# Optimization experiments

Measured on AMD Instinct MI355X. Metric: run time of the kernel, lower is better.

The kernel has to match this reference:

```python
import jax, jax.numpy as jnp
import numpy as np

B, N, C, H = 2, 2048, 128, 4
C4 = C // 4


def setup_inputs() -> dict:
    key = jax.random.key(0)
    ks = jax.random.split(key, 20)
    s = 0.02
    f = lambda k, sh: (jax.random.normal(k, sh, jnp.float32) * s)
    return {
        'x': jax.random.normal(ks[0], (B, N, C), jnp.float32),
        'A': jax.random.randint(ks[1], (N, N), 0, 2).astype(jnp.int32),
        'q_w1': f(ks[2], (C, C)), 'kv_w1': f(ks[3], (2 * C, C)),
        'proj_w1': f(ks[4], (C, C)), 'proj_b1': jnp.zeros((C,), jnp.float32),
        'q_w2': f(ks[5], (C, C)), 'kv_w2': f(ks[6], (2 * C, C)),
        'proj_w2': f(ks[7], (C, C)), 'proj_b2': jnp.zeros((C,), jnp.float32),
        'cq_w': f(ks[8], (C4, C)), 'cq_b': jnp.zeros((C4,), jnp.float32),
        'ck_w': f(ks[9], (C4, C)), 'ck_b': jnp.zeros((C4,), jnp.float32),
        'cv_w': f(ks[10], (C, C)), 'cv_b': jnp.zeros((C,), jnp.float32),
        'gc_w': f(ks[11], (C, C)), 'gc_b': jnp.zeros((C,), jnp.float32),
    }


def _attn_block(x, A, qw, kvw, pw, pb):
    # Attention._inner_attention + residual; qkv_bias=False, scale=head_dim**-0.5
    b, n, c = x.shape
    hd = c // H
    q = (x @ qw.T).reshape(b, n, H, hd).transpose(0, 2, 1, 3)          # [B,H,N,hd]
    kv = (x @ kvw.T).reshape(b, n, 2, H, hd).transpose(2, 0, 3, 1, 4)  # [2,B,H,N,hd]
    k, v = kv[0], kv[1]
    attn = jnp.einsum('bhnd,bhmd->bhnm', q, k) * (hd ** -0.5)
    attn = jnp.where(A[None, None] > 0, attn, jnp.float32(-9e15))
    attn = jax.nn.softmax(attn, axis=-1)
    out = jnp.einsum('bhnm,bhmd->bhnd', attn, v).transpose(0, 2, 1, 3).reshape(b, n, c)
    return out @ pw.T + pb + x


def _graph_conv(x, cq_w, cq_b, ck_w, ck_b, cv_w, cv_b, gc_w, gc_b):
    # GraphConvolution.forward: conv1d(k=1) QKV, softmax, topk scatter mask, masked softmax, bmm
    b, s, c = x.shape
    xp = x.transpose(0, 2, 1)                                          # [B,C,N]
    query = jnp.einsum('oi,bin->bon', cq_w, xp) + cq_b[:, None]        # [B,C/4,N]
    keyt = (jnp.einsum('oi,bin->bon', ck_w, xp) + ck_b[:, None]).transpose(0, 2, 1)  # [B,N,C/4]
    adj = jax.nn.softmax(jnp.einsum('bnc,bcm->bnm', keyt, query), axis=-1)           # [B,N,N]
    kk = int(s / 3 * 2)                                                # top-2/3 per row
    _, idx = jax.lax.top_k(adj, kk)                                    # [B,N,kk]
    mask = jnp.zeros(adj.shape, bool).at[
        jnp.arange(b)[:, None, None], jnp.arange(s)[None, :, None], idx].set(True)
    adj = jax.nn.softmax(jnp.where(mask, adj, -jnp.inf), axis=-1)
    value = (jnp.einsum('oi,bin->bon', cv_w, xp) + cv_b[:, None]).transpose(0, 2, 1)  # [B,N,C]
    support = value @ gc_w
    return jnp.einsum('bnm,bmc->bnc', adj, support) + gc_b


def reference(x, A, q_w1, kv_w1, proj_w1, proj_b1, q_w2, kv_w2, proj_w2, proj_b2,
              cq_w, cq_b, ck_w, ck_b, cv_w, cv_b, gc_w, gc_b):
    x = _attn_block(x, A, q_w1, kv_w1, proj_w1, proj_b1)
    x = _attn_block(x, A, q_w2, kv_w2, proj_w2, proj_b2)
    return _graph_conv(x, cq_w, cq_b, ck_w, ck_b, cv_w, cv_b, gc_w, gc_b)
```

## Files before the change

### kernel.cpp

```cpp
#include <hip/hip_runtime.h>
#include <hip/hip_bf16.h>
#include <math.h>

#define BB 2
#define NN 2048
#define CC 128
#define HH 4
#define HD 32
#define KK_TOP 1365

typedef __attribute__((ext_vector_type(8))) short v8s;
typedef __attribute__((ext_vector_type(4))) float f32x4;

#define MFMA16(a, b, c) __builtin_amdgcn_mfma_f32_16x16x32_bf16(a, b, c, 0, 0, 0)

__device__ inline float wave_max_f(float v) {
    #pragma unroll
    for (int m = 1; m < 64; m <<= 1) v = fmaxf(v, __shfl_xor(v, m));
    return v;
}
__device__ inline float wave_min_f(float v) {
    #pragma unroll
    for (int m = 1; m < 64; m <<= 1) v = fminf(v, __shfl_xor(v, m));
    return v;
}
__device__ inline float wave_sum_f(float v) {
    #pragma unroll
    for (int m = 1; m < 64; m <<= 1) v += __shfl_xor(v, m);
    return v;
}
__device__ inline unsigned short bf16bits(float x) {
    __hip_bfloat16 h = __float2bfloat16(x);
    return *reinterpret_cast<unsigned short*>(&h);
}

__global__ __launch_bounds__(256) void prep_k(
    const int* __restrict__ A, unsigned* __restrict__ Ab2,
    const float* __restrict__ cv_w, const float* __restrict__ cv_b,
    const float* __restrict__ gc_w, float* __restrict__ MT, float* __restrict__ B2)
{
    const int bx = blockIdx.x;
    if (bx < 512) {
        const int lane = threadIdx.x & 63;
        const int w = threadIdx.x >> 6;
        const int row = bx * 4 + w;
        const int* rp = A + (size_t)row * 2048;
        for (int i = 0; i < 32; ++i) {
            unsigned long long bal = __ballot(rp[i * 64 + lane] > 0);
            if (lane == 0)  Ab2[(size_t)row * 64 + 2 * i]     = (unsigned)bal;
            if (lane == 32) Ab2[(size_t)row * 64 + 2 * i + 1] = (unsigned)(bal >> 32);
        }
    } else {
        const int b2 = bx - 512;
        const int c = b2 * 2 + (threadIdx.x >> 7);
        const int k = threadIdx.x & 127;
        float a = 0.f;
        #pragma unroll 4
        for (int i = 0; i < 128; ++i)
            a += cv_w[(size_t)i * 128 + k] * gc_w[(size_t)i * 128 + c];
        MT[(size_t)c * 128 + k] = a;
        if (b2 == 0 && threadIdx.x < 128) {
            float s = 0.f;
            #pragma unroll 4
            for (int i = 0; i < 128; ++i)
                s += cv_b[i] * gc_w[(size_t)i * 128 + threadIdx.x];
            B2[threadIdx.x] = s;
        }
    }
}

enum { MODE_QKV = 0, MODE_PROJ = 1 };

template <int MODE>
__global__ __launch_bounds__(256) void gemm128_k(
    const float* __restrict__ X, const float* __restrict__ W0,
    const float* __restrict__ W1, const float* __restrict__ bias,
    const float* __restrict__ resid, void* __restrict__ out0v,
    void* __restrict__ out1v, void* __restrict__ out2v)
{
    __shared__ __align__(16) float Xs[64][132];
    __shared__ __align__(16) float Ws[32][132];
    const int tid = threadIdx.x;
    const int m0 = blockIdx.x * 64;
    const int n0 = blockIdx.y * 32;

    #pragma unroll
    for (int i = 0; i < 32; ++i) {
        int idx = tid + i * 256;
        int row = idx >> 7, col = idx & 127;
        Xs[row][col] = X[(size_t)(m0 + row) * 128 + col];
    }
    #pragma unroll
    for (int i = 0; i < 16; ++i) {
        int idx = tid + i * 256;
        int r = idx >> 7, col = idx & 127;
        int gr = n0 + r;
        const float* wp;
        if (MODE == MODE_QKV)
            wp = (gr < 128) ? (W0 + (size_t)gr * 128) : (W1 + (size_t)(gr - 128) * 128);
        else
            wp = W0 + (size_t)gr * 128;
        Ws[r][col] = wp[col];
    }
    __syncthreads();

    const int r = tid >> 4;
    const int c = tid & 15;
    float acc[4][2] = {{0.f, 0.f}, {0.f, 0.f}, {0.f, 0.f}, {0.f, 0.f}};

    #pragma unroll
    for (int k = 0; k < 128; k += 4) {
        float4 w0 = *(const float4*)&Ws[c][k];
        float4 w1 = *(const float4*)&Ws[c + 16][k];
        #pragma unroll
        for (int i = 0; i < 4; ++i) {
            float4 xv = *(const float4*)&Xs[r + 16 * i][k];
            acc[i][0] += xv.x * w0.x + xv.y * w0.y + xv.z * w0.z + xv.w * w0.w;
            acc[i][1] += xv.x * w1.x + xv.y * w1.y + xv.z * w1.z + xv.w * w1.w;
        }
    }

    #pragma unroll
    for (int i = 0; i < 4; ++i) {
        int m = m0 + r + 16 * i;
        int b = m >> 11, n = m & 2047;
        #pragma unroll
        for (int jj = 0; jj < 2; ++jj) {
            int ccol = n0 + c + 16 * jj;
            float v = acc[i][jj];
            if (MODE == MODE_QKV) {
                __hip_bfloat16 hv = __float2bfloat16(v);
                if (ccol < 128) {
                    int hh = ccol >> 5, d = ccol & 31;
                    ((__hip_bfloat16*)out0v)[((size_t)(b * 4 + hh) * 2048 + n) * 32 + d] = hv;
                } else if (ccol < 256) {
                    int c2 = ccol - 128; int hh = c2 >> 5, d = c2 & 31;
                    ((__hip_bfloat16*)out1v)[((size_t)(b * 4 + hh) * 2048 + n) * 32 + d] = hv;
                } else {
                    int c2 = ccol - 256; int hh = c2 >> 5, d = c2 & 31;
                    ((__hip_bfloat16*)out2v)[((size_t)(b * 4 + hh) * 32 + d) * 2048 + n] = hv;
                }
            } else {
                ((float*)out0v)[(size_t)m * 128 + ccol] = v + bias[ccol] + resid[(size_t)m * 128 + ccol];
            }
        }
    }
}

__global__ __launch_bounds__(256) void graphmm_k(
    const float* __restrict__ X, const float* __restrict__ cq_w,
    const float* __restrict__ cq_b, const float* __restrict__ ck_w,
    const float* __restrict__ ck_b, const float* __restrict__ MT,
    const float* __restrict__ B2, float* __restrict__ QgT,
    float* __restrict__ Kg, __hip_bfloat16* __restrict__ SUPt)
{
    __shared__ __align__(16) float Xs[64][132];
    __shared__ __align__(16) float Ws[32][132];
    const int tid = threadIdx.x;
    const int m0 = blockIdx.x * 64;
    const int y = blockIdx.y;
    const float* W0   = (y == 0) ? cq_w : (y == 1) ? ck_w : MT;
    const float* bias = (y == 0) ? cq_b : (y == 1) ? ck_b : B2;
    const int n0 = (y < 2) ? 0 : (y - 2) * 32;

    #pragma unroll
    for (int i = 0; i < 32; ++i) {
        int idx = tid + i * 256;
        int row = idx >> 7, col = idx & 127;
        Xs[row][col] = X[(size_t)(m0 + row) * 128 + col];
    }
    #pragma unroll
    for (int i = 0; i < 16; ++i) {
        int idx = tid + i * 256;
        int r = idx >> 7, col = idx & 127;
        Ws[r][col] = W0[(size_t)(n0 + r) * 128 + col];
    }
    __syncthreads();

    const int r = tid >> 4;
    const int c = tid & 15;
    float acc[4][2] = {{0.f, 0.f}, {0.f, 0.f}, {0.f, 0.f}, {0.f, 0.f}};

    #pragma unroll
    for (int k = 0; k < 128; k += 4) {
        float4 w0 = *(const float4*)&Ws[c][k];
        float4 w1 = *(const float4*)&Ws[c + 16][k];
        #pragma unroll
        for (int i = 0; i < 4; ++i) {
            float4 xv = *(const float4*)&Xs[r + 16 * i][k];
            acc[i][0] += xv.x * w0.x + xv.y * w0.y + xv.z * w0.z + xv.w * w0.w;
            acc[i][1] += xv.x * w1.x + xv.y * w1.y + xv.z * w1.z + xv.w * w1.w;
        }
    }

    #pragma unroll
    for (int i = 0; i < 4; ++i) {
        int m = m0 + r + 16 * i;
        int b = m >> 11, n = m & 2047;
        #pragma unroll
        for (int jj = 0; jj < 2; ++jj) {
            int ccol = n0 + c + 16 * jj;
            float v = acc[i][jj];
            if (y == 0) {
                QgT[((size_t)b * 32 + ccol) * 2048 + n] = v + bias[ccol];
            } else if (y == 1) {
                Kg[(size_t)m * 32 + ccol] = v + bias[ccol];
            } else {
                SUPt[((size_t)b * 128 + ccol) * 2048 + n] = __float2bfloat16(v + bias[ccol]);
            }
        }
    }
}

__global__ __launch_bounds__(512, 8) void attn_mfma_k(
    const short* __restrict__ Qb, const short* __restrict__ Kb,
    const short* __restrict__ Vt, const unsigned* __restrict__ Ab2,
    float* __restrict__ O)
{
    __shared__ __align__(16) float OLDS[8][64][8];
    __shared__ float lred[8][16];

    const int tid = threadIdx.x;
    const int w = tid >> 6, lane = tid & 63;
    const int g = lane >> 4, c = lane & 15;
    const int bb = 4 * g;
    const int wg = blockIdx.x;
    const int b = wg >> 9, h = (wg >> 7) & 3, r0w = (wg & 127) << 4;
    const int bh = b * 4 + h;

    const v8s qf = *(const v8s*)(Qb + ((size_t)bh * 2048 + r0w + c) * 32 + g * 8);
    const short* Kp = Kb + (size_t)bh * 2048 * 32;
    const short* Vp = Vt + (size_t)bh * 32 * 2048;
    const unsigned* Mrow = Ab2 + (size_t)(r0w + c) * 64;

    f32x4 o0 = {0.f, 0.f, 0.f, 0.f}, o1 = {0.f, 0.f, 0.f, 0.f};
    float lsum = 0.f;
    const float SC2 = 0.25503487f;
    const bool lo = (g < 2);
    const int aA = (32 * (g & 1) + c) * 4;
    const int aB = aA + 64;

    #pragma unroll 2
    for (int t = 0; t < 8; ++t) {
        const int kt = t * 8 + w;
        const int key0 = kt * 32;
        v8s kf0 = *(const v8s*)(Kp + (size_t)(key0 + c) * 32 + g * 8);
        v8s kf1 = *(const v8s*)(Kp + (size_t)(key0 + 16 + c) * 32 + g * 8);
        unsigned mw = Mrow[kt];
        const f32x4 z = {0.f, 0.f, 0.f, 0.f};
        f32x4 s0 = MFMA16(kf0, qf, z);
        f32x4 s1 = MFMA16(kf1, qf, z);

        float p0[4], p1[4];
        #pragma unroll
        for (int r = 0; r < 4; ++r) {
            p0[r] = ((mw >> (bb + r)) & 1u)      ? exp2f(s0[r] * SC2) : 0.f;
            p1[r] = ((mw >> (16 + bb + r)) & 1u) ? exp2f(s1[r] * SC2) : 0.f;
        }
        lsum += p0[0] + p0[1] + p0[2] + p0[3] + p1[0] + p1[1] + p1[2] + p1[3];

        int w00 = (int)bf16bits(p0[0]) | ((int)bf16bits(p0[1]) << 16);
        int w01 = (int)bf16bits(p0[2]) | ((int)bf16bits(p0[3]) << 16);
        int w10 = (int)bf16bits(p1[0]) | ((int)bf16bits(p1[1]) << 16);
        int w11 = (int)bf16bits(p1[2]) | ((int)bf16bits(p1[3]) << 16);

        int e0, e1;
        union { int wv[4]; v8s v; } pf;
        e0 = __builtin_amdgcn_ds_bpermute(aA, w00);
        e1 = __builtin_amdgcn_ds_bpermute(aA, w10);
        pf.wv[0] = lo ? e0 : e1;
        e0 = __builtin_amdgcn_ds_bpermute(aA, w01);
        e1 = __builtin_amdgcn_ds_bpermute(aA, w11);
        pf.wv[1] = lo ? e0 : e1;
        e0 = __builtin_amdgcn_ds_bpermute(aB, w00);
        e1 = __builtin_amdgcn_ds_bpermute(aB, w10);
        pf.wv[2] = lo ? e0 : e1;
        e0 = __builtin_amdgcn_ds_bpermute(aB, w01);
        e1 = __builtin_amdgcn_ds_bpermute(aB, w11);
        pf.wv[3] = lo ? e0 : e1;

        v8s vf0 = *(const v8s*)(Vp + (size_t)c * 2048 + key0 + g * 8);
        v8s vf1 = *(const v8s*)(Vp + (size_t)(16 + c) * 2048 + key0 + g * 8);
        o0 = MFMA16(pf.v, vf0, o0);
        o1 = MFMA16(pf.v, vf1, o1);
    }

    lsum += __shfl_xor(lsum, 16);
    lsum += __shfl_xor(lsum, 32);

    *(f32x4*)&OLDS[w][lane][0] = o0;
    *(f32x4*)&OLDS[w][lane][4] = o1;
    if (lane < 16) lred[w][lane] = lsum;
    __syncthreads();

    if (tid < 64) {
        float iv[4];
        #pragma unroll
        for (int r = 0; r < 4; ++r) {
            float s = lred[0][bb + r];
            #pragma unroll
            for (int ww = 1; ww < 8; ++ww) s += lred[ww][bb + r];
            iv[r] = 1.f / s;
        }
        f32x4 a0 = *(f32x4*)&OLDS[0][lane][0];
        f32x4 a1 = *(f32x4*)&OLDS[0][lane][4];
        #pragma unroll
        for (int ww = 1; ww < 8; ++ww) {
            a0 += *(f32x4*)&OLDS[ww][lane][0];
            a1 += *(f32x4*)&OLDS[ww][lane][4];
        }
        #pragma unroll
        for (int r = 0; r < 4; ++r) {
            size_t base = ((size_t)b * 2048 + r0w + bb + r) * 128 + h * 32;
            O[base + c]      = a0[r] * iv[r];
            O[base + 16 + c] = a1[r] * iv[r];
        }
    }
}

__global__ __launch_bounds__(512, 4) void gadjtopk_k(
    const float* __restrict__ Kg, const float* __restrict__ QgT,
    __hip_bfloat16* __restrict__ ADJb)
{
    __shared__ float kg_s[8][32];
    __shared__ float scores[8][2048];

    const int tid = threadIdx.x;
    const int wg = blockIdx.x;
    const int b = wg >> 8;
    const int r0 = (wg & 255) << 3;

    if (tid < 256) {
        int rr = tid >> 5, d = tid & 31;
        kg_s[rr][d] = Kg[((size_t)b * 2048 + r0 + rr) * 32 + d];
    }
    __syncthreads();

    const float* Qp = QgT + (size_t)b * 32 * 2048;
    float acc[8][4];
    #pragma unroll
    for (int rr = 0; rr < 8; ++rr)
        #pragma unroll
        for (int s = 0; s < 4; ++s) acc[rr][s] = 0.f;

    for (int dd = 0; dd < 32; ++dd) {
        float qv[8];
        #pragma unroll
        for (int rr = 0; rr < 8; ++rr) qv[rr] = kg_s[rr][dd];
        const float* kp = Qp + (size_t)dd * 2048 + tid;
        #pragma unroll
        for (int s = 0; s < 4; ++s) {
            float kv = kp[s * 512];
            #pragma unroll
            for (int rr = 0; rr < 8; ++rr)
                acc[rr][s] = fmaf(qv[rr], kv, acc[rr][s]);
        }
    }
    #pragma unroll
    for (int s = 0; s < 4; ++s) {
        int jj = tid + 512 * s;
        #pragma unroll
        for (int rr = 0; rr < 8; ++rr) scores[rr][jj] = acc[rr][s];
    }
    __syncthreads();

    const int lane = tid & 63, w = tid >> 6;

    float mx = -3.0e38f;
    #pragma unroll
    for (int i = 0; i < 32; ++i) mx = fmaxf(mx, scores[w][lane + i * 64]);
    mx = wave_max_f(mx);

    float sm0 = 0.f;
    #pragma unroll
    for (int i = 0; i < 32; ++i) {
        float p = expf(scores[w][lane + i * 64] - mx);
        scores[w][lane + i * 64] = p;
        sm0 += p;
    }
    sm0 = wave_sum_f(sm0);
    const float ivw = 1.f / sm0;

    unsigned k_[32];
    float mxp = 0.f, mnp = 3.0e38f;
    #pragma unroll
    for (int i = 0; i < 32; ++i) {
        float p = scores[w][lane + i * 64] * ivw;
        k_[i] = __float_as_uint(p);
        mxp = fmaxf(mxp, p);
        mnp = fminf(mnp, p);
    }
    mxp = wave_max_f(mxp);
    mnp = wave_min_f(mnp);

    unsigned thr = __float_as_uint(mnp);
    const unsigned umax = __float_as_uint(mxp);
    const unsigned diff = thr ^ umax;
    if (diff != 0u) {
        const int hb = 31 - __builtin_clz(diff);
        thr = (umax >> (hb + 1)) << (hb + 1);
        for (int bit = hb; bit >= 0; --bit) {
            unsigned cand = thr | (1u << bit);
            int cnt = 0;
            #pragma unroll
            for (int i = 0; i < 32; ++i)
                cnt += (int)__popcll(__ballot(k_[i] >= cand));
            if (cnt == KK_TOP) { thr = cand; break; }
            if (cnt > KK_TOP) thr = cand;
        }
    }

    int gt_c = 0;
    #pragma unroll
    for (int i = 0; i < 32; ++i)
        gt_c += (int)__popcll(__ballot(k_[i] > thr));
    const int need = KK_TOP - gt_c;

    unsigned keepmask = 0u;
    int running = 0;
    const unsigned long long ltmask = (lane == 0) ? 0ull : (~0ull >> (64 - lane));
    #pragma unroll
    for (int i = 0; i < 32; ++i) {
        bool tie = (k_[i] == thr);
        unsigned long long bal = __ballot(tie);
        int before = running + (int)__popcll(bal & ltmask);
        bool keep = (k_[i] > thr) || (tie && before < need);
        running += (int)__popcll(bal);
        if (keep) keepmask |= (1u << i);
    }

    const float LOG2E = 1.4426950408889634f;
    float sm = 0.f;
    #pragma unroll
    for (int i = 0; i < 32; ++i)
        if ((keepmask >> i) & 1u)
            sm += exp2f((__uint_as_float(k_[i]) - mxp) * LOG2E);
    sm = wave_sum_f(sm);
    const float ivs = 1.f / sm;

    __hip_bfloat16* rp = ADJb + (size_t)(b * 2048 + r0 + w) * 2048;
    #pragma unroll
    for (int i = 0; i < 32; ++i) {
        float o = ((keepmask >> i) & 1u)
                    ? exp2f((__uint_as_float(k_[i]) - mxp) * LOG2E) * ivs : 0.f;
        rp[lane + i * 64] = __float2bfloat16(o);
    }
}

__global__ __launch_bounds__(512, 8) void outgemm_mfma_k(
    const short* __restrict__ ADJb, const short* __restrict__ SUPt,
    const float* __restrict__ gcb, float* __restrict__ OUT)
{
    __shared__ __align__(16) float OL[8][64][16];
    const int tid = threadIdx.x;
    const int w = tid >> 6, lane = tid & 63;
    const int g = lane >> 4, c = lane & 15;
    const int r0w = blockIdx.x * 16;
    const int n0 = blockIdx.y * 64;
    const int b = r0w >> 11;
    const short* Bp = SUPt + (size_t)b * 128 * 2048;

    f32x4 acc[4];
    #pragma unroll
    for (int f = 0; f < 4; ++f) acc[f] = (f32x4){0.f, 0.f, 0.f, 0.f};

    #pragma unroll 2
    for (int i = 0; i < 8; ++i) {
        const int k0 = w * 256 + i * 32;
        v8s af = *(const v8s*)(ADJb + (size_t)(r0w + c) * 2048 + k0 + g * 8);
        #pragma unroll
        for (int f = 0; f < 4; ++f) {
            v8s bf_ = *(const v8s*)(Bp + (size_t)(n0 + f * 16 + c) * 2048 + k0 + g * 8);
            acc[f] = MFMA16(af, bf_, acc[f]);
        }
    }

    #pragma unroll
    for (int f = 0; f < 4; ++f) *(f32x4*)&OL[w][lane][f * 4] = acc[f];
    __syncthreads();

    #pragma unroll
    for (int u = 0; u < 2; ++u) {
        int idx = tid + u * 512;
        int ls = idx >> 4, s = idx & 15;
        float v = OL[0][ls][s];
        #pragma unroll
        for (int ww = 1; ww < 8; ++ww) v += OL[ww][ls][s];
        int f = s >> 2, r = s & 3;
        int row = r0w + 4 * (ls >> 4) + r;
        int col = n0 + f * 16 + (ls & 15);
        OUT[(size_t)row * 128 + col] = v + gcb[col];
    }
}

extern "C" void kernel_launch(void* const* d_in, const int* in_sizes, int n_in,
                              void* d_out, int out_size, void* d_ws, size_t ws_size,
                              hipStream_t stream)
{
    const float* x       = (const float*)d_in[0];
    const int*   A       = (const int*)d_in[1];
    const float* q_w1    = (const float*)d_in[2];
    const float* kv_w1   = (const float*)d_in[3];
    const float* proj_w1 = (const float*)d_in[4];
    const float* proj_b1 = (const float*)d_in[5];
    const float* q_w2    = (const float*)d_in[6];
    const float* kv_w2   = (const float*)d_in[7];
    const float* proj_w2 = (const float*)d_in[8];
    const float* proj_b2 = (const float*)d_in[9];
    const float* cq_w    = (const float*)d_in[10];
    const float* cq_b    = (const float*)d_in[11];
    const float* ck_w    = (const float*)d_in[12];
    const float* ck_b    = (const float*)d_in[13];
    const float* cv_w    = (const float*)d_in[14];
    const float* cv_b    = (const float*)d_in[15];
    const float* gc_w    = (const float*)d_in[16];
    const float* gc_b    = (const float*)d_in[17];
    float* out = (float*)d_out;

    char* ws = (char*)d_ws;
    __hip_bfloat16* Qb   = (__hip_bfloat16*)(ws + 0);
    __hip_bfloat16* Kb   = (__hip_bfloat16*)(ws + 1048576);
    __hip_bfloat16* Vt   = (__hip_bfloat16*)(ws + 2097152);
    __hip_bfloat16* ADJb = (__hip_bfloat16*)(ws + 3145728);
    unsigned*       Ab2  = (unsigned*)      (ws + 19922944);
    float*          O    = (float*)         (ws + 20447232);
    float*          X1   = (float*)         (ws + 22544384);
    float*          X2   = (float*)         (ws + 24641536);
    float*          QgT  = (float*)         (ws + 26738688);
    float*          Kg   = (float*)         (ws + 27262976);
    __hip_bfloat16* SUPt = (__hip_bfloat16*)(ws + 27787264);
    float*          MT   = (float*)         (ws + 28835840);
    float*          B2   = (float*)         (ws + 28901376);

    dim3 blk(256);
    dim3 blk512(512);

    hipLaunchKernelGGL(prep_k, dim3(576), blk, 0, stream, A, Ab2, cv_w, cv_b, gc_w, MT, B2);

    hipLaunchKernelGGL((gemm128_k<MODE_QKV>), dim3(64, 12), blk, 0, stream,
                       x, q_w1, kv_w1, nullptr, nullptr, Qb, Kb, Vt);
    hipLaunchKernelGGL(attn_mfma_k, dim3(1024), blk512, 0, stream,
                       (const short*)Qb, (const short*)Kb, (const short*)Vt, Ab2, O);
    hipLaunchKernelGGL((gemm128_k<MODE_PROJ>), dim3(64, 4), blk, 0, stream,
                       O, proj_w1, nullptr, proj_b1, x, X1, nullptr, nullptr);

    hipLaunchKernelGGL((gemm128_k<MODE_QKV>), dim3(64, 12), blk, 0, stream,
                       X1, q_w2, kv_w2, nullptr, nullptr, Qb, Kb, Vt);
    hipLaunchKernelGGL(attn_mfma_k, dim3(1024), blk512, 0, stream,
                       (const short*)Qb, (const short*)Kb, (const short*)Vt, Ab2, O);
    hipLaunchKernelGGL((gemm128_k<MODE_PROJ>), dim3(64, 4), blk, 0, stream,
                       O, proj_w2, nullptr, proj_b2, X1, X2, nullptr, nullptr);

    hipLaunchKernelGGL(graphmm_k, dim3(64, 6), blk, 0, stream,
                       X2, cq_w, cq_b, ck_w, ck_b, MT, B2, QgT, Kg, SUPt);
    hipLaunchKernelGGL(gadjtopk_k, dim3(512), blk512, 0, stream, Kg, QgT, ADJb);
    hipLaunchKernelGGL(outgemm_mfma_k, dim3(256, 2), blk512, 0, stream,
                       (const short*)ADJb, (const short*)SUPt, gc_b, out);
}
```

Measured before the change: 286.6 us.

## Replace FP32 SIMT projection GEMMs with bf16 MFMA GEMMs and bf16 intermediates

The QKV and output-projection GEMMs in both attention blocks now use 16x16x32 bf16 MFMA instructions instead of FP32 scalar FMAs through shared memory. The input x and all attention weights are converted to bf16 in the prep kernel. The attention output and the first residual stream are also emitted in bf16 so they can feed the next MFMA GEMM directly. This cuts ALU time and memory traffic for the dense projections, at the cost of lower precision and extra conversion work in the prep kernel.

```diff
diff --git a/kernel.cpp b/kernel.cpp
--- a/kernel.cpp
+++ b/kernel.cpp
@@ -37,7 +37,12 @@
 __global__ __launch_bounds__(256) void prep_k(
     const int* __restrict__ A, unsigned* __restrict__ Ab2,
     const float* __restrict__ cv_w, const float* __restrict__ cv_b,
-    const float* __restrict__ gc_w, float* __restrict__ MT, float* __restrict__ B2)
+    const float* __restrict__ gc_w, float* __restrict__ MT, float* __restrict__ B2,
+    const float* __restrict__ x, short* __restrict__ xb,
+    const float* __restrict__ q_w1, const float* __restrict__ kv_w1,
+    const float* __restrict__ proj_w1, const float* __restrict__ q_w2,
+    const float* __restrict__ kv_w2, const float* __restrict__ proj_w2,
+    short* __restrict__ WALLb)
 {
     const int bx = blockIdx.x;
     if (bx < 512) {
@@ -50,7 +55,7 @@
             if (lane == 0)  Ab2[(size_t)row * 64 + 2 * i]     = (unsigned)bal;
             if (lane == 32) Ab2[(size_t)row * 64 + 2 * i + 1] = (unsigned)(bal >> 32);
         }
-    } else {
+    } else if (bx < 576) {
         const int b2 = bx - 512;
         const int c = b2 * 2 + (threadIdx.x >> 7);
         const int k = threadIdx.x & 127;
@@ -66,82 +71,80 @@
                 s += cv_b[i] * gc_w[(size_t)i * 128 + threadIdx.x];
             B2[threadIdx.x] = s;
         }
+    } else if (bx < 640) {
+        const size_t base = (size_t)(bx - 576) * 8192;
+        #pragma unroll 8
+        for (int i = 0; i < 32; ++i) {
+            size_t e = base + threadIdx.x + i * 256;
+            xb[e] = (short)bf16bits(x[e]);
+        }
+    } else {
+        const int base = (bx - 640) * 8192;
+        const float* src; int off;
+        if (base < 16384)       { src = q_w1;    off = base; }
+        else if (base < 49152)  { src = kv_w1;   off = base - 16384; }
+        else if (base < 65536)  { src = proj_w1; off = base - 49152; }
+        else if (base < 81920)  { src = q_w2;    off = base - 65536; }
+        else if (base < 114688) { src = kv_w2;   off = base - 81920; }
+        else                    { src = proj_w2; off = base - 114688; }
+        short* dst = WALLb + base;
+        #pragma unroll 8
+        for (int i = 0; i < 32; ++i) {
+            int e = threadIdx.x + i * 256;
+            dst[e] = (short)bf16bits(src[off + e]);
+        }
     }
 }
 
 enum { MODE_QKV = 0, MODE_PROJ = 1 };
 
-template <int MODE>
-__global__ __launch_bounds__(256) void gemm128_k(
-    const float* __restrict__ X, const float* __restrict__ W0,
-    const float* __restrict__ W1, const float* __restrict__ bias,
-    const float* __restrict__ resid, void* __restrict__ out0v,
-    void* __restrict__ out1v, void* __restrict__ out2v)
-{
-    __shared__ __align__(16) float Xs[64][132];
-    __shared__ __align__(16) float Ws[32][132];
+template <int MODE, bool EMITB>
+__global__ __launch_bounds__(256) void mfma_gemm_k(
+    const short* __restrict__ Xb, const short* __restrict__ Wb,
+    const float* __restrict__ bias, const float* __restrict__ resid,
+    short* __restrict__ Qo, short* __restrict__ Ko, short* __restrict__ Vto,
+    float* __restrict__ Fo, short* __restrict__ Bo)
+{
     const int tid = threadIdx.x;
-    const int m0 = blockIdx.x * 64;
-    const int n0 = blockIdx.y * 32;
-
-    #pragma unroll
-    for (int i = 0; i < 32; ++i) {
-        int idx = tid + i * 256;
-        int row = idx >> 7, col = idx & 127;
-        Xs[row][col] = X[(size_t)(m0 + row) * 128 + col];
-    }
-    #pragma unroll
-    for (int i = 0; i < 16; ++i) {
-        int idx = tid + i * 256;
-        int r = idx >> 7, col = idx & 127;
-        int gr = n0 + r;
-        const float* wp;
-        if (MODE == MODE_QKV)
-            wp = (gr < 128) ? (W0 + (size_t)gr * 128) : (W1 + (size_t)(gr - 128) * 128);
-        else
-            wp = W0 + (size_t)gr * 128;
-        Ws[r][col] = wp[col];
-    }
-    __syncthreads();
-
-    const int r = tid >> 4;
-    const int c = tid & 15;
-    float acc[4][2] = {{0.f, 0.f}, {0.f, 0.f}, {0.f, 0.f}, {0.f, 0.f}};
-
-    #pragma unroll
-    for (int k = 0; k < 128; k += 4) {
-        float4 w0 = *(const float4*)&Ws[c][k];
-        float4 w1 = *(const float4*)&Ws[c + 16][k];
-        #pragma unroll
-        for (int i = 0; i < 4; ++i) {
-            float4 xv = *(const float4*)&Xs[r + 16 * i][k];
-            acc[i][0] += xv.x * w0.x + xv.y * w0.y + xv.z * w0.z + xv.w * w0.w;
-            acc[i][1] += xv.x * w1.x + xv.y * w1.y + xv.z * w1.z + xv.w * w1.w;
-        }
-    }
-
-    #pragma unroll
-    for (int i = 0; i < 4; ++i) {
-        int m = m0 + r + 16 * i;
-        int b = m >> 11, n = m & 2047;
-        #pragma unroll
-        for (int jj = 0; jj < 2; ++jj) {
-            int ccol = n0 + c + 16 * jj;
-            float v = acc[i][jj];
+    const int w = tid >> 6, lane = tid & 63;
+    const int g = lane >> 4, c = lane & 15;
+    const int m0 = blockIdx.x * 64 + w * 16;
+    const int nbase = blockIdx.y * 64;
+
+    v8s af[4];
+    #pragma unroll
+    for (int kk = 0; kk < 4; ++kk)
+        af[kk] = *(const v8s*)(Xb + (size_t)(m0 + c) * 128 + kk * 32 + g * 8);
+
+    for (int nf = 0; nf < 4; ++nf) {
+        const int n0 = nbase + nf * 16;
+        f32x4 acc = {0.f, 0.f, 0.f, 0.f};
+        #pragma unroll
+        for (int kk = 0; kk < 4; ++kk) {
+            v8s bfr = *(const v8s*)(Wb + (size_t)(n0 + c) * 128 + kk * 32 + g * 8);
+            acc = MFMA16(af[kk], bfr, acc);
+        }
+        const int ccol = n0 + c;
+        #pragma unroll
+        for (int r = 0; r < 4; ++r) {
+            const int m = m0 + 4 * g + r;
+            const int b = m >> 11, n = m & 2047;
             if (MODE == MODE_QKV) {
-                __hip_bfloat16 hv = __float2bfloat16(v);
+                unsigned short hv = bf16bits(acc[r]);
                 if (ccol < 128) {
                     int hh = ccol >> 5, d = ccol & 31;
-                    ((__hip_bfloat16*)out0v)[((size_t)(b * 4 + hh) * 2048 + n) * 32 + d] = hv;
+                    Qo[((size_t)(b * 4 + hh) * 2048 + n) * 32 + d] = (short)hv;
                 } else if (ccol < 256) {
                     int c2 = ccol - 128; int hh = c2 >> 5, d = c2 & 31;
-                    ((__hip_bfloat16*)out1v)[((size_t)(b * 4 + hh) * 2048 + n) * 32 + d] = hv;
+                    Ko[((size_t)(b * 4 + hh) * 2048 + n) * 32 + d] = (short)hv;
                 } else {
                     int c2 = ccol - 256; int hh = c2 >> 5, d = c2 & 31;
-                    ((__hip_bfloat16*)out2v)[((size_t)(b * 4 + hh) * 32 + d) * 2048 + n] = hv;
+                    Vto[((size_t)(b * 4 + hh) * 32 + d) * 2048 + n] = (short)hv;
                 }
             } else {
-                ((float*)out0v)[(size_t)m * 128 + ccol] = v + bias[ccol] + resid[(size_t)m * 128 + ccol];
+                float v = acc[r] + bias[ccol] + resid[(size_t)m * 128 + ccol];
+                Fo[(size_t)m * 128 + ccol] = v;
+                if (EMITB) Bo[(size_t)m * 128 + ccol] = (short)bf16bits(v);
             }
         }
     }
@@ -215,7 +218,7 @@
 __global__ __launch_bounds__(512, 8) void attn_mfma_k(
     const short* __restrict__ Qb, const short* __restrict__ Kb,
     const short* __restrict__ Vt, const unsigned* __restrict__ Ab2,
-    float* __restrict__ O)
+    short* __restrict__ Ob)
 {
     __shared__ __align__(16) float OLDS[8][64][8];
     __shared__ float lred[8][16];
@@ -312,8 +315,8 @@
         #pragma unroll
         for (int r = 0; r < 4; ++r) {
             size_t base = ((size_t)b * 2048 + r0w + bb + r) * 128 + h * 32;
-            O[base + c]      = a0[r] * iv[r];
-            O[base + 16 + c] = a1[r] * iv[r];
+            Ob[base + c]      = (short)bf16bits(a0[r] * iv[r]);
+            Ob[base + 16 + c] = (short)bf16bits(a1[r] * iv[r]);
         }
     }
 }
@@ -518,38 +521,43 @@
     float* out = (float*)d_out;
 
     char* ws = (char*)d_ws;
-    __hip_bfloat16* Qb   = (__hip_bfloat16*)(ws + 0);
-    __hip_bfloat16* Kb   = (__hip_bfloat16*)(ws + 1048576);
-    __hip_bfloat16* Vt   = (__hip_bfloat16*)(ws + 2097152);
+    short*          Qb   = (short*)         (ws + 0);
+    short*          Kb   = (short*)         (ws + 1048576);
+    short*          Vt   = (short*)         (ws + 2097152);
     __hip_bfloat16* ADJb = (__hip_bfloat16*)(ws + 3145728);
     unsigned*       Ab2  = (unsigned*)      (ws + 19922944);
-    float*          O    = (float*)         (ws + 20447232);
-    float*          X1   = (float*)         (ws + 22544384);
+    short*          Ob   = (short*)         (ws + 20447232);
+    float*          X1   = (float*)         (ws + 21495808);
+    short*          X1b  = (short*)         (ws + 23592960);
     float*          X2   = (float*)         (ws + 24641536);
     float*          QgT  = (float*)         (ws + 26738688);
     float*          Kg   = (float*)         (ws + 27262976);
     __hip_bfloat16* SUPt = (__hip_bfloat16*)(ws + 27787264);
     float*          MT   = (float*)         (ws + 28835840);
     float*          B2   = (float*)         (ws + 28901376);
+    short*          xb   = (short*)         (ws + 28901888);
+    short*          WALLb= (short*)         (ws + 29950464);
 
     dim3 blk(256);
     dim3 blk512(512);
 
-    hipLaunchKernelGGL(prep_k, dim3(576), blk, 0, stream, A, Ab2, cv_w, cv_b, gc_w, MT, B2);
-
-    hipLaunchKernelGGL((gemm128_k<MODE_QKV>), dim3(64, 12), blk, 0, stream,
-                       x, q_w1, kv_w1, nullptr, nullptr, Qb, Kb, Vt);
+    hipLaunchKernelGGL(prep_k, dim3(656), blk, 0, stream,
+                       A, Ab2, cv_w, cv_b, gc_w, MT, B2,
+                       x, xb, q_w1, kv_w1, proj_w1, q_w2, kv_w2, proj_w2, WALLb);
+
+    hipLaunchKernelGGL((mfma_gemm_k<MODE_QKV, false>), dim3(64, 6), blk, 0, stream,
+                       xb, WALLb, nullptr, nullptr, Qb, Kb, Vt, nullptr, nullptr);
     hipLaunchKernelGGL(attn_mfma_k, dim3(1024), blk512, 0, stream,
-                       (const short*)Qb, (const short*)Kb, (const short*)Vt, Ab2, O);
-    hipLaunchKernelGGL((gemm128_k<MODE_PROJ>), dim3(64, 4), blk, 0, stream,
-                       O, proj_w1, nullptr, proj_b1, x, X1, nullptr, nullptr);
-
-    hipLaunchKernelGGL((gemm128_k<MODE_QKV>), dim3(64, 12), blk, 0, stream,
-                       X1, q_w2, kv_w2, nullptr, nullptr, Qb, Kb, Vt);
+                       Qb, Kb, Vt, Ab2, Ob);
+    hipLaunchKernelGGL((mfma_gemm_k<MODE_PROJ, true>), dim3(64, 2), blk, 0, stream,
+                       Ob, WALLb + 49152, proj_b1, x, nullptr, nullptr, nullptr, X1, X1b);
+
+    hipLaunchKernelGGL((mfma_gemm_k<MODE_QKV, false>), dim3(64, 6), blk, 0, stream,
+                       X1b, WALLb + 65536, nullptr, nullptr, Qb, Kb, Vt, nullptr, nullptr);
     hipLaunchKernelGGL(attn_mfma_k, dim3(1024), blk512, 0, stream,
-                       (const short*)Qb, (const short*)Kb, (const short*)Vt, Ab2, O);
-    hipLaunchKernelGGL((gemm128_k<MODE_PROJ>), dim3(64, 4), blk, 0, stream,
-                       O, proj_w2, nullptr, proj_b2, X1, X2, nullptr, nullptr);
+                       Qb, Kb, Vt, Ab2, Ob);
+    hipLaunchKernelGGL((mfma_gemm_k<MODE_PROJ, false>), dim3(64, 2), blk, 0, stream,
+                       Ob, WALLb + 114688, proj_b2, X1, nullptr, nullptr, nullptr, X2, nullptr);
 
     hipLaunchKernelGGL(graphmm_k, dim3(64, 6), blk, 0, stream,
                        X2, cq_w, cq_b, ck_w, ck_b, MT, B2, QgT, Kg, SUPt);
```

New measurement: 277.9 us. 3.1% less time.
